# Kernel tuning notes

Hardware: AMD Instinct MI355X
Metric: run time of the kernel (lower is better)

The kernel has to match this reference:

```python
import jax, jax.numpy as jnp
import numpy as np

IN_FEATURES = 4096
OUT_FEATURES = 4096
N_GROUPS = 32
GROUP_SIZE = IN_FEATURES // N_GROUPS  # 128


def setup_inputs() -> dict:
    key = jax.random.key(0)
    k_x, k_qw, k_s, k_zp, k_b = jax.random.split(key, 5)
    x = jax.random.normal(k_x, (2, 2048, IN_FEATURES), dtype=jnp.float32)
    # 4-bit GPTQ quantized weight values in [0, 16)
    qweight_int = jax.random.randint(k_qw, (IN_FEATURES, OUT_FEATURES), 0, 16, dtype=jnp.int32)
    scales = jax.random.uniform(k_s, (N_GROUPS, OUT_FEATURES), dtype=jnp.float32, minval=0.001, maxval=0.02)
    zero_points = jax.random.randint(k_zp, (N_GROUPS, OUT_FEATURES), 0, 16, dtype=jnp.int32)
    # standard (non-permuted) g_idx: group index per input channel
    g_idx = (jnp.arange(IN_FEATURES, dtype=jnp.int32) // GROUP_SIZE).astype(jnp.int32)
    bias = jax.random.normal(k_b, (OUT_FEATURES,), dtype=jnp.float32)
    return {"x": x, "qweight_int": qweight_int, "scales": scales,
            "zero_points": zero_points, "g_idx": g_idx, "bias": bias}


def reference(x, qweight_int, scales, zero_points, g_idx, bias):
    dtype = x.dtype
    gi = g_idx.astype(jnp.int32)
    # dequantize: W[i, o] = scales[g_idx[i], o] * (q[i, o] - zp[g_idx[i], o])
    qw = qweight_int.astype(dtype)                       # [in, out]
    zp = zero_points.astype(dtype)[gi]                   # [in, out] via gather
    sc = scales.astype(dtype)[gi]                        # [in, out] via gather
    weight = sc * (qw - zp)                              # [in, out]
    out_shape = x.shape[:-1] + (qweight_int.shape[1],)
    x2d = x.reshape(-1, x.shape[-1])                     # [tokens, in]
    out = (x2d @ weight).reshape(out_shape)              # [b, s, out]
    out = out + bias.astype(dtype)
    return out
```

## Files before the change

### kernel.cpp

```cpp
#include <hip/hip_runtime.h>
#include <hip/hip_bf16.h>

typedef int  int4v  __attribute__((ext_vector_type(4)));
typedef int  int16v __attribute__((ext_vector_type(16)));

#define M_DIM 4096
#define N_DIM 4096
#define K_DIM 4096
#define NG 32
#define GS 128

__global__ void prep_kernel(const float* __restrict__ x,
                            signed char* __restrict__ xq,
                            float* __restrict__ sx,
                            const int* __restrict__ qw,
                            const int* __restrict__ zps,
                            signed char* __restrict__ wq) {
    __shared__ float red[4];
    __shared__ float inv_s;
    const int tid = threadIdx.x;
    if (blockIdx.x < 4096) {
        const int m = blockIdx.x;
        const float4* xr = reinterpret_cast<const float4*>(x + (long)m * K_DIM);
        float4 v[4];
        float amax = 0.f;
#pragma unroll
        for (int j = 0; j < 4; ++j) {
            v[j] = xr[tid * 4 + j];
            amax = fmaxf(amax, fmaxf(fmaxf(fabsf(v[j].x), fabsf(v[j].y)),
                                     fmaxf(fabsf(v[j].z), fabsf(v[j].w))));
        }
#pragma unroll
        for (int off = 32; off >= 1; off >>= 1)
            amax = fmaxf(amax, __shfl_xor(amax, off));
        if ((tid & 63) == 0) red[tid >> 6] = amax;
        __syncthreads();
        if (tid == 0) {
            float a = fmaxf(fmaxf(red[0], red[1]), fmaxf(red[2], red[3]));
            sx[m] = a * (1.f / 127.f);
            inv_s = (a > 0.f) ? 127.f / a : 0.f;
        }
        __syncthreads();
        const float inv = inv_s;
        unsigned p[4];
#pragma unroll
        for (int j = 0; j < 4; ++j) {
            int a0 = __float2int_rn(v[j].x * inv);
            int a1 = __float2int_rn(v[j].y * inv);
            int a2 = __float2int_rn(v[j].z * inv);
            int a3 = __float2int_rn(v[j].w * inv);
            p[j] = (a0 & 255) | ((a1 & 255) << 8) | ((a2 & 255) << 16) | ((a3 & 255) << 24);
        }
        *reinterpret_cast<uint4*>(xq + (long)m * K_DIM + tid * 16) =
            make_uint4(p[0], p[1], p[2], p[3]);
        return;
    }
    const int bx = blockIdx.x - 4096;
    const int n0 = (bx & 63) * 64;
    const int k0 = (bx >> 6) * 64;
    const int g  = k0 >> 7;
    const int n  = tid & 63;
    const int w  = tid >> 6;
    const int zp = zps[g * N_DIM + n0 + n];
    const int kk = k0 + w * 16;
    unsigned p[4];
#pragma unroll
    for (int c = 0; c < 4; ++c) {
        unsigned acc = 0;
#pragma unroll
        for (int j = 0; j < 4; ++j) {
            int q = qw[(long)(kk + c * 4 + j) * N_DIM + n0 + n];
            acc |= (unsigned)((q - zp) & 255) << (8 * j);
        }
        p[c] = acc;
    }
    *reinterpret_cast<uint4*>(wq + (long)(n0 + n) * K_DIM + kk) =
        make_uint4(p[0], p[1], p[2], p[3]);
}

#define BM 256
#define BN 256
#define BK 128
#define NT (K_DIM / BK)

__device__ __forceinline__ void async_ld16(const signed char* g, const signed char* l) {
    __builtin_amdgcn_global_load_lds(
        (const __attribute__((address_space(1))) void*)g,
        (__attribute__((address_space(3))) void*)l, 16, 0, 0);
}

__device__ __forceinline__ void stage_tiles(const signed char* agp, const signed char* bgp,
                                            signed char* asb, signed char* bsb,
                                            int wave, int kk) {
#pragma unroll
    for (int p = 0; p < 4; ++p)
        async_ld16(agp + (long)(p * 64) * K_DIM + kk, asb + p * 8192 + wave * 1024);
#pragma unroll
    for (int p = 0; p < 4; ++p)
        async_ld16(bgp + (long)(p * 64) * K_DIM + kk, bsb + p * 8192 + wave * 1024);
}

__global__ __launch_bounds__(512, 1) void gemm_kernel(
    const signed char* __restrict__ A,
    const signed char* __restrict__ Bq,
    const float* __restrict__ scales,
    const float* __restrict__ sx,
    const float* __restrict__ bias,
    float* __restrict__ C) {
    __shared__ signed char As[2][BM * BK];
    __shared__ signed char Bs[2][BN * BK];
    const int tid  = threadIdx.x;
    const int wave = tid >> 6;
    const int lane = tid & 63;
    const int half = lane >> 5;
    const int l32  = lane & 31;
    const int wm = (wave >> 2) * 128;
    const int wn = (wave & 3) * 64;

    const int bid = (int)blockIdx.x;
    const int swz = (bid & 7) * 32 + (bid >> 3);
    const int m0 = (swz >> 4) * BM;
    const int n0 = (swz & 15) * BN;

    const int srow  = tid >> 3;
    const int sunit = (tid & 7) ^ (srow & 7);
    const signed char* agp = A  + (long)(m0 + srow) * K_DIM + sunit * 16;
    const signed char* bgp = Bq + (long)(n0 + srow) * K_DIM + sunit * 16;
    const float* sp = scales + n0 + wn + l32;

    float facc[4][2][16];
#pragma unroll
    for (int mt = 0; mt < 4; ++mt)
#pragma unroll
        for (int nt = 0; nt < 2; ++nt)
#pragma unroll
            for (int r = 0; r < 16; ++r) facc[mt][nt][r] = 0.f;
    int16v zero16;
#pragma unroll
    for (int r = 0; r < 16; ++r) zero16[r] = 0;

    stage_tiles(agp, bgp, As[0], Bs[0], wave, 0);
    float s0 = sp[0];
    float s1 = sp[32];
    __syncthreads();

    for (int t = 0; t < NT; ++t) {
        if (t + 1 < NT)
            stage_tiles(agp, bgp, As[(t + 1) & 1], Bs[(t + 1) & 1], wave, (t + 1) * BK);
        float ns0 = 0.f, ns1 = 0.f;
        if (t + 1 < NT) {
            ns0 = sp[(long)(t + 1) * N_DIM];
            ns1 = sp[(long)(t + 1) * N_DIM + 32];
        }

        const signed char* Ab = As[t & 1];
        const signed char* Bb = Bs[t & 1];
        int4v bf[2][4];
#pragma unroll
        for (int nt = 0; nt < 2; ++nt) {
            int n = wn + nt * 32 + l32;
#pragma unroll
            for (int ks = 0; ks < 4; ++ks) {
                int slot = (2 * ks + half) ^ (n & 7);
                bf[nt][ks] = *reinterpret_cast<const int4v*>(&Bb[n * BK + slot * 16]);
            }
        }
#pragma unroll
        for (int mt = 0; mt < 4; ++mt) {
            int m = wm + mt * 32 + l32;
            int4v af[4];
#pragma unroll
            for (int ks = 0; ks < 4; ++ks) {
                int slot = (2 * ks + half) ^ (m & 7);
                af[ks] = *reinterpret_cast<const int4v*>(&Ab[m * BK + slot * 16]);
            }
            int16v c0 = __builtin_amdgcn_mfma_i32_32x32x32_i8(af[0], bf[0][0], zero16, 0, 0, 0);
            int16v c1 = __builtin_amdgcn_mfma_i32_32x32x32_i8(af[0], bf[1][0], zero16, 0, 0, 0);
#pragma unroll
            for (int ks = 1; ks < 4; ++ks) {
                c0 = __builtin_amdgcn_mfma_i32_32x32x32_i8(af[ks], bf[0][ks], c0, 0, 0, 0);
                c1 = __builtin_amdgcn_mfma_i32_32x32x32_i8(af[ks], bf[1][ks], c1, 0, 0, 0);
            }
#pragma unroll
            for (int r = 0; r < 16; ++r) {
                facc[mt][0][r] += s0 * (float)c0[r];
                facc[mt][1][r] += s1 * (float)c1[r];
            }
        }
        __syncthreads();
        s0 = ns0;
        s1 = ns1;
    }

    float bv[2];
    bv[0] = bias[n0 + wn + l32];
    bv[1] = bias[n0 + wn + 32 + l32];
    const int rowh = half * 4;
#pragma unroll
    for (int mt = 0; mt < 4; ++mt) {
#pragma unroll
        for (int r = 0; r < 16; ++r) {
            int row = (r & 3) + 8 * (r >> 2) + rowh;
            int gm  = m0 + wm + mt * 32 + row;
            float sxm = sx[gm];
            float* crow = C + (long)gm * N_DIM + n0 + wn;
            crow[l32]      = facc[mt][0][r] * sxm + bv[0];
            crow[32 + l32] = facc[mt][1][r] * sxm + bv[1];
        }
    }
}

extern "C" void kernel_launch(void* const* d_in, const int* in_sizes, int n_in,
                              void* d_out, int out_size, void* d_ws, size_t ws_size,
                              hipStream_t stream) {
    const float* x      = (const float*)d_in[0];
    const int*   qw     = (const int*)d_in[1];
    const float* scales = (const float*)d_in[2];
    const int*   zps    = (const int*)d_in[3];
    const float* bias   = (const float*)d_in[5];
    float* out = (float*)d_out;

    signed char* xq = (signed char*)d_ws;
    signed char* wq = (signed char*)d_ws + (size_t)M_DIM * K_DIM;
    float*       sx = (float*)((signed char*)d_ws + 2 * (size_t)M_DIM * K_DIM);

    prep_kernel<<<8192, 256, 0, stream>>>(x, xq, sx, qw, zps, wq);
    gemm_kernel<<<N_DIM / BN * (M_DIM / BM), 512, 0, stream>>>(
        xq, wq, scales, sx, bias, out);
}
```

Measured before the change: 266.2 us.

## Interleave async tile prefetch with MFMA phases and transpose weights via LDS

The GEMM main loop is split into four phases, one per M sub-tile. Each phase issues a quarter of the next tile's global-to-LDS loads, then crosses a workgroup barrier and runs its MFMAs at raised wave priority, so memory traffic is spread across the compute instead of issued in one burst. The weight prep kernel now reads qweight and zero points with coalesced 16-byte vector loads and transposes through a swizzled LDS tile, replacing strided scalar global reads. The extra per-phase barriers add synchronisation cost and could stall waves if loads and compute do not overlap as intended.

```diff
diff --git a/kernel.cpp b/kernel.cpp
--- a/kernel.cpp
+++ b/kernel.cpp
@@ -16,10 +16,10 @@
                             const int* __restrict__ qw,
                             const int* __restrict__ zps,
                             signed char* __restrict__ wq) {
-    __shared__ float red[4];
-    __shared__ float inv_s;
     const int tid = threadIdx.x;
     if (blockIdx.x < 4096) {
+        __shared__ float red[4];
+        __shared__ float inv_s;
         const int m = blockIdx.x;
         const float4* xr = reinterpret_cast<const float4*>(x + (long)m * K_DIM);
         float4 v[4];
@@ -55,27 +55,43 @@
             make_uint4(p[0], p[1], p[2], p[3]);
         return;
     }
+    __shared__ signed char lt[128 * 32];
     const int bx = blockIdx.x - 4096;
-    const int n0 = (bx & 63) * 64;
-    const int k0 = (bx >> 6) * 64;
-    const int g  = k0 >> 7;
-    const int n  = tid & 63;
-    const int w  = tid >> 6;
-    const int zp = zps[g * N_DIM + n0 + n];
-    const int kk = k0 + w * 16;
-    unsigned p[4];
+    const int n0 = (bx & 127) * 32;
+    const int k0 = (bx >> 7) * 128;
+    const int g  = bx >> 7;
+    const int kl = tid >> 1;
+    const int h  = tid & 1;
+    int4 qv[4], zv[4];
 #pragma unroll
     for (int c = 0; c < 4; ++c) {
-        unsigned acc = 0;
-#pragma unroll
-        for (int j = 0; j < 4; ++j) {
-            int q = qw[(long)(kk + c * 4 + j) * N_DIM + n0 + n];
-            acc |= (unsigned)((q - zp) & 255) << (8 * j);
-        }
-        p[c] = acc;
-    }
-    *reinterpret_cast<uint4*>(wq + (long)(n0 + n) * K_DIM + kk) =
-        make_uint4(p[0], p[1], p[2], p[3]);
+        qv[c] = *reinterpret_cast<const int4*>(&qw[(long)(k0 + kl) * N_DIM + n0 + h * 16 + c * 4]);
+        zv[c] = *reinterpret_cast<const int4*>(&zps[(long)g * N_DIM + n0 + h * 16 + c * 4]);
+    }
+    {
+        const int swz = ((kl >> 3) & 7) << 2;
+        int* ltw = reinterpret_cast<int*>(lt);
+#pragma unroll
+        for (int c = 0; c < 4; ++c) {
+            unsigned d = (unsigned)((qv[c].x - zv[c].x) & 255)
+                       | ((unsigned)((qv[c].y - zv[c].y) & 255) << 8)
+                       | ((unsigned)((qv[c].z - zv[c].z) & 255) << 16)
+                       | ((unsigned)((qv[c].w - zv[c].w) & 255) << 24);
+            ltw[(kl * 32 + ((h * 16 + c * 4) ^ swz)) >> 2] = d;
+        }
+    }
+    __syncthreads();
+    const int nl = tid >> 3;
+    const int kq = tid & 7;
+    unsigned acc[4] = {0u, 0u, 0u, 0u};
+#pragma unroll
+    for (int j = 0; j < 16; ++j) {
+        const int kr = kq * 16 + j;
+        unsigned by = (unsigned char)lt[kr * 32 + (nl ^ (((kr >> 3) & 7) << 2))];
+        acc[j >> 2] |= by << (8 * (j & 3));
+    }
+    *reinterpret_cast<uint4*>(wq + (long)(n0 + nl) * K_DIM + k0 + kq * 16) =
+        make_uint4(acc[0], acc[1], acc[2], acc[3]);
 }
 
 #define BM 256
@@ -89,15 +105,41 @@
         (__attribute__((address_space(3))) void*)l, 16, 0, 0);
 }
 
-__device__ __forceinline__ void stage_tiles(const signed char* agp, const signed char* bgp,
-                                            signed char* asb, signed char* bsb,
-                                            int wave, int kk) {
-#pragma unroll
-    for (int p = 0; p < 4; ++p)
-        async_ld16(agp + (long)(p * 64) * K_DIM + kk, asb + p * 8192 + wave * 1024);
-#pragma unroll
-    for (int p = 0; p < 4; ++p)
-        async_ld16(bgp + (long)(p * 64) * K_DIM + kk, bsb + p * 8192 + wave * 1024);
+__device__ __forceinline__ int16v mf(const int4v a, const int4v b, const int16v c) {
+    return __builtin_amdgcn_mfma_i32_32x32x32_i8(a, b, c, 0, 0, 0);
+}
+
+__device__ __forceinline__ void read_af(const signed char* Ab, int wm, int mt,
+                                        int l32, int half, int4v af[4]) {
+    const int m = wm + mt * 32 + l32;
+#pragma unroll
+    for (int ks = 0; ks < 4; ++ks) {
+        const int slot = (2 * ks + half) ^ (m & 7);
+        af[ks] = *reinterpret_cast<const int4v*>(&Ab[m * BK + slot * 16]);
+    }
+}
+
+__device__ __forceinline__ void mfma_phase(const int4v af[4], const int4v bf[2][4],
+                                           int16v& c0, int16v& c1) {
+    int16v z;
+#pragma unroll
+    for (int r = 0; r < 16; ++r) z[r] = 0;
+    c0 = mf(af[0], bf[0][0], z);
+    c1 = mf(af[0], bf[1][0], z);
+#pragma unroll
+    for (int ks = 1; ks < 4; ++ks) {
+        c0 = mf(af[ks], bf[0][ks], c0);
+        c1 = mf(af[ks], bf[1][ks], c1);
+    }
+}
+
+__device__ __forceinline__ void rescale(const int16v& c0, const int16v& c1,
+                                        float s0, float s1, float* f0, float* f1) {
+#pragma unroll
+    for (int r = 0; r < 16; ++r) {
+        f0[r] += s0 * (float)c0[r];
+        f1[r] += s1 * (float)c1[r];
+    }
 }
 
 __global__ __launch_bounds__(512, 1) void gemm_kernel(
@@ -135,61 +177,90 @@
         for (int nt = 0; nt < 2; ++nt)
 #pragma unroll
             for (int r = 0; r < 16; ++r) facc[mt][nt][r] = 0.f;
-    int16v zero16;
-#pragma unroll
-    for (int r = 0; r < 16; ++r) zero16[r] = 0;
-
-    stage_tiles(agp, bgp, As[0], Bs[0], wave, 0);
-    float s0 = sp[0];
-    float s1 = sp[32];
+
+#pragma unroll
+    for (int p = 0; p < 4; ++p)
+        async_ld16(agp + (long)(p * 64) * K_DIM, As[0] + p * 8192 + wave * 1024);
+#pragma unroll
+    for (int p = 0; p < 4; ++p)
+        async_ld16(bgp + (long)(p * 64) * K_DIM, Bs[0] + p * 8192 + wave * 1024);
     __syncthreads();
 
     for (int t = 0; t < NT; ++t) {
-        if (t + 1 < NT)
-            stage_tiles(agp, bgp, As[(t + 1) & 1], Bs[(t + 1) & 1], wave, (t + 1) * BK);
-        float ns0 = 0.f, ns1 = 0.f;
-        if (t + 1 < NT) {
-            ns0 = sp[(long)(t + 1) * N_DIM];
-            ns1 = sp[(long)(t + 1) * N_DIM + 32];
-        }
-
         const signed char* Ab = As[t & 1];
         const signed char* Bb = Bs[t & 1];
+        signed char* Anx = As[(t + 1) & 1];
+        signed char* Bnx = Bs[(t + 1) & 1];
+        const bool pf = (t + 1 < NT);
+        const long kn = (long)(t + 1) * BK;
         int4v bf[2][4];
+        int4v af[4];
+        int16v c0, c1;
+
 #pragma unroll
         for (int nt = 0; nt < 2; ++nt) {
-            int n = wn + nt * 32 + l32;
+            const int n = wn + nt * 32 + l32;
 #pragma unroll
             for (int ks = 0; ks < 4; ++ks) {
-                int slot = (2 * ks + half) ^ (n & 7);
+                const int slot = (2 * ks + half) ^ (n & 7);
                 bf[nt][ks] = *reinterpret_cast<const int4v*>(&Bb[n * BK + slot * 16]);
             }
         }
-#pragma unroll
-        for (int mt = 0; mt < 4; ++mt) {
-            int m = wm + mt * 32 + l32;
-            int4v af[4];
-#pragma unroll
-            for (int ks = 0; ks < 4; ++ks) {
-                int slot = (2 * ks + half) ^ (m & 7);
-                af[ks] = *reinterpret_cast<const int4v*>(&Ab[m * BK + slot * 16]);
-            }
-            int16v c0 = __builtin_amdgcn_mfma_i32_32x32x32_i8(af[0], bf[0][0], zero16, 0, 0, 0);
-            int16v c1 = __builtin_amdgcn_mfma_i32_32x32x32_i8(af[0], bf[1][0], zero16, 0, 0, 0);
-#pragma unroll
-            for (int ks = 1; ks < 4; ++ks) {
-                c0 = __builtin_amdgcn_mfma_i32_32x32x32_i8(af[ks], bf[0][ks], c0, 0, 0, 0);
-                c1 = __builtin_amdgcn_mfma_i32_32x32x32_i8(af[ks], bf[1][ks], c1, 0, 0, 0);
-            }
-#pragma unroll
-            for (int r = 0; r < 16; ++r) {
-                facc[mt][0][r] += s0 * (float)c0[r];
-                facc[mt][1][r] += s1 * (float)c1[r];
-            }
-        }
+        read_af(Ab, wm, 0, l32, half, af);
+        if (pf) {
+            async_ld16(agp + kn, Anx + wave * 1024);
+            async_ld16(agp + (long)64 * K_DIM + kn, Anx + 8192 + wave * 1024);
+        }
+        const float s0c = sp[(long)t * N_DIM];
+        const float s1c = sp[(long)t * N_DIM + 32];
+        __builtin_amdgcn_sched_barrier(0);
+        __builtin_amdgcn_s_barrier();
+        __builtin_amdgcn_sched_barrier(0);
+        __builtin_amdgcn_s_setprio(1);
+        mfma_phase(af, bf, c0, c1);
+        __builtin_amdgcn_s_setprio(0);
+
+        rescale(c0, c1, s0c, s1c, facc[0][0], facc[0][1]);
+        read_af(Ab, wm, 1, l32, half, af);
+        if (pf) {
+            async_ld16(agp + (long)128 * K_DIM + kn, Anx + 16384 + wave * 1024);
+            async_ld16(agp + (long)192 * K_DIM + kn, Anx + 24576 + wave * 1024);
+        }
+        __builtin_amdgcn_sched_barrier(0);
+        __builtin_amdgcn_s_barrier();
+        __builtin_amdgcn_sched_barrier(0);
+        __builtin_amdgcn_s_setprio(1);
+        mfma_phase(af, bf, c0, c1);
+        __builtin_amdgcn_s_setprio(0);
+
+        rescale(c0, c1, s0c, s1c, facc[1][0], facc[1][1]);
+        read_af(Ab, wm, 2, l32, half, af);
+        if (pf) {
+            async_ld16(bgp + kn, Bnx + wave * 1024);
+            async_ld16(bgp + (long)64 * K_DIM + kn, Bnx + 8192 + wave * 1024);
+        }
+        __builtin_amdgcn_sched_barrier(0);
+        __builtin_amdgcn_s_barrier();
+        __builtin_amdgcn_sched_barrier(0);
+        __builtin_amdgcn_s_setprio(1);
+        mfma_phase(af, bf, c0, c1);
+        __builtin_amdgcn_s_setprio(0);
+
+        rescale(c0, c1, s0c, s1c, facc[2][0], facc[2][1]);
+        read_af(Ab, wm, 3, l32, half, af);
+        if (pf) {
+            async_ld16(bgp + (long)128 * K_DIM + kn, Bnx + 16384 + wave * 1024);
+            async_ld16(bgp + (long)192 * K_DIM + kn, Bnx + 24576 + wave * 1024);
+        }
+        __builtin_amdgcn_sched_barrier(0);
+        __builtin_amdgcn_s_barrier();
+        __builtin_amdgcn_sched_barrier(0);
+        __builtin_amdgcn_s_setprio(1);
+        mfma_phase(af, bf, c0, c1);
+        __builtin_amdgcn_s_setprio(0);
+
+        rescale(c0, c1, s0c, s1c, facc[3][0], facc[3][1]);
         __syncthreads();
-        s0 = ns0;
-        s1 = ns1;
     }
 
     float bv[2];
@@ -200,9 +271,9 @@
     for (int mt = 0; mt < 4; ++mt) {
 #pragma unroll
         for (int r = 0; r < 16; ++r) {
-            int row = (r & 3) + 8 * (r >> 2) + rowh;
-            int gm  = m0 + wm + mt * 32 + row;
-            float sxm = sx[gm];
+            const int row = (r & 3) + 8 * (r >> 2) + rowh;
+            const int gm  = m0 + wm + mt * 32 + row;
+            const float sxm = sx[gm];
             float* crow = C + (long)gm * N_DIM + n0 + wn;
             crow[l32]      = facc[mt][0][r] * sxm + bv[0];
             crow[32 + l32] = facc[mt][1][r] * sxm + bv[1];
```

After: 272.5 us. 1.02x slower.
